# Kernel optimization log

Measured on AMD Instinct MI355X. Metric: run time of the kernel, lower is better.

## Reference

```python
import jax, jax.numpy as jnp
import numpy as np

K = 5
PAD = 2


def setup_inputs() -> dict:
    key = jax.random.key(0)
    k1, k2 = jax.random.split(key)
    B, C, H, W = 8, 4, 256, 256
    x = jax.random.normal(k1, (B, C, H, W), dtype=jnp.float32)
    filt = jax.random.uniform(k2, (B, C * K * K, H, W), dtype=jnp.float32)
    return {"x": x, "filt": filt}


def reference(x, filt):
    B, C, H, W = x.shape
    # identity kernel: out channel j of each group picks the j-th position of the kxk window
    eye = jnp.eye(K * K, dtype=x.dtype).reshape(K * K, 1, K, K)
    kernel = jnp.tile(eye, (C, 1, 1, 1))  # [C*K^2, 1, K, K], grouped conv = per-channel patch expand
    x_localexpand = jax.lax.conv_general_dilated(
        x, kernel,
        window_strides=(1, 1),
        padding=[(PAD, PAD), (PAD, PAD)],
        dimension_numbers=("NCHW", "OIHW", "NCHW"),
        feature_group_count=C,
    )  # [B, C*K^2, H, W]
    y = jnp.tanh(jnp.sum(x_localexpand * filt, axis=1, keepdims=True))  # [B,1,H,W]
    return y
```

## Files before the change

kernel.cpp:

```cpp
#include <hip/hip_runtime.h>
#include <math.h>

#define Hd 256
#define Wd 256
#define Cc 4
#define Kk 5

__global__ __launch_bounds__(256) void dynf_kernel(const float* __restrict__ x,
                                                   const float* __restrict__ filt,
                                                   float* __restrict__ out) {
    int t  = blockIdx.x * blockDim.x + threadIdx.x;
    int w4 = t & 63;
    int h  = (t >> 6) & 255;
    int b  = t >> 14;
    int w0 = w4 << 2;

    const size_t HW = (size_t)Hd * Wd;
    const float* xb = x + (size_t)b * Cc * HW;
    const float* fb = filt + (size_t)b * (Cc * Kk * Kk) * HW;

    float acc0 = 0.f, acc1 = 0.f, acc2 = 0.f, acc3 = 0.f;

    for (int c = 0; c < Cc; ++c) {
        const float* xc = xb + (size_t)c * HW;
        #pragma unroll
        for (int di = 0; di < Kk; ++di) {
            int hh = h + di - 2;
            if (hh < 0 || hh >= Hd) continue;
            const float* xr = xc + (size_t)hh * Wd;

            float4 left  = (w0 >= 4)      ? *(const float4*)(xr + w0 - 4) : make_float4(0.f,0.f,0.f,0.f);
            float4 mid   =                  *(const float4*)(xr + w0);
            float4 right = (w0 + 4 < Wd)  ? *(const float4*)(xr + w0 + 4) : make_float4(0.f,0.f,0.f,0.f);
            float xrow[8];
            xrow[0] = left.z;  xrow[1] = left.w;
            xrow[2] = mid.x;   xrow[3] = mid.y;  xrow[4] = mid.z;  xrow[5] = mid.w;
            xrow[6] = right.x; xrow[7] = right.y;

            const float* fr = fb + ((size_t)(c * (Kk*Kk) + di * Kk)) * HW + (size_t)h * Wd + w0;
            #pragma unroll
            for (int dj = 0; dj < Kk; ++dj) {
                float4 f = *(const float4*)(fr + (size_t)dj * HW);
                acc0 = fmaf(xrow[dj + 0], f.x, acc0);
                acc1 = fmaf(xrow[dj + 1], f.y, acc1);
                acc2 = fmaf(xrow[dj + 2], f.z, acc2);
                acc3 = fmaf(xrow[dj + 3], f.w, acc3);
            }
        }
    }

    float4 o;
    o.x = tanhf(acc0); o.y = tanhf(acc1); o.z = tanhf(acc2); o.w = tanhf(acc3);
    *(float4*)(out + (size_t)b * HW + (size_t)h * Wd + w0) = o;
}

extern "C" void kernel_launch(void* const* d_in, const int* in_sizes, int n_in,
                              void* d_out, int out_size, void* d_ws, size_t ws_size,
                              hipStream_t stream) {
    const float* x    = (const float*)d_in[0];
    const float* filt = (const float*)d_in[1];
    float* out        = (float*)d_out;

    const int total_threads = 8 * 256 * 64;
    const int block = 256;
    const int grid  = total_threads / block;
    dynf_kernel<<<grid, block, 0, stream>>>(x, filt, out);
}
```

Baseline: 286.3 us.

## Split channels across waves per row block and reduce via shared memory

```diff
diff --git a/kernel.cpp b/kernel.cpp
--- a/kernel.cpp
+++ b/kernel.cpp
@@ -4,54 +4,63 @@
 #define Hd 256
 #define Wd 256
 #define Cc 4
-#define Kk 5
+#define KK 5
 
-__global__ __launch_bounds__(256) void dynf_kernel(const float* __restrict__ x,
-                                                   const float* __restrict__ filt,
-                                                   float* __restrict__ out) {
-    int t  = blockIdx.x * blockDim.x + threadIdx.x;
-    int w4 = t & 63;
-    int h  = (t >> 6) & 255;
-    int b  = t >> 14;
-    int w0 = w4 << 2;
+typedef float v4f __attribute__((ext_vector_type(4)));
+
+__global__ __launch_bounds__(256, 4) void dynf_kernel(const float* __restrict__ x,
+                                                      const float* __restrict__ filt,
+                                                      float* __restrict__ out) {
+    const int bh   = blockIdx.x;
+    const int b    = bh >> 8;
+    const int h    = bh & 255;
+    const int c    = threadIdx.x >> 6;
+    const int lane = threadIdx.x & 63;
+    const int w0   = lane << 2;
 
     const size_t HW = (size_t)Hd * Wd;
-    const float* xb = x + (size_t)b * Cc * HW;
-    const float* fb = filt + (size_t)b * (Cc * Kk * Kk) * HW;
+    const float* xc = x + ((size_t)b * Cc + c) * HW;
+    const float* fb = filt + ((size_t)(b * (Cc * KK * KK) + c * (KK * KK))) * HW
+                      + (size_t)h * Wd + w0;
 
-    float acc0 = 0.f, acc1 = 0.f, acc2 = 0.f, acc3 = 0.f;
+    float a0 = 0.f, a1 = 0.f, a2 = 0.f, a3 = 0.f;
+    const v4f vzero = {0.f, 0.f, 0.f, 0.f};
 
-    for (int c = 0; c < Cc; ++c) {
-        const float* xc = xb + (size_t)c * HW;
-        #pragma unroll
-        for (int di = 0; di < Kk; ++di) {
-            int hh = h + di - 2;
-            if (hh < 0 || hh >= Hd) continue;
+    #pragma unroll
+    for (int di = 0; di < KK; ++di) {
+        const int hh = h + di - 2;
+        if (hh >= 0 && hh < Hd) {
             const float* xr = xc + (size_t)hh * Wd;
+            v4f left  = *(const v4f*)(xr + (w0 ? (w0 - 4) : 0));
+            v4f mid   = *(const v4f*)(xr + w0);
+            v4f right = *(const v4f*)(xr + ((w0 + 4 < Wd) ? (w0 + 4) : 0));
+            if (w0 == 0)      left  = vzero;
+            if (w0 + 4 >= Wd) right = vzero;
+            float xrow[8] = {left.z, left.w, mid.x, mid.y, mid.z, mid.w, right.x, right.y};
 
-            float4 left  = (w0 >= 4)      ? *(const float4*)(xr + w0 - 4) : make_float4(0.f,0.f,0.f,0.f);
-            float4 mid   =                  *(const float4*)(xr + w0);
-            float4 right = (w0 + 4 < Wd)  ? *(const float4*)(xr + w0 + 4) : make_float4(0.f,0.f,0.f,0.f);
-            float xrow[8];
-            xrow[0] = left.z;  xrow[1] = left.w;
-            xrow[2] = mid.x;   xrow[3] = mid.y;  xrow[4] = mid.z;  xrow[5] = mid.w;
-            xrow[6] = right.x; xrow[7] = right.y;
-
-            const float* fr = fb + ((size_t)(c * (Kk*Kk) + di * Kk)) * HW + (size_t)h * Wd + w0;
+            const float* fr = fb + (size_t)(di * KK) * HW;
             #pragma unroll
-            for (int dj = 0; dj < Kk; ++dj) {
-                float4 f = *(const float4*)(fr + (size_t)dj * HW);
-                acc0 = fmaf(xrow[dj + 0], f.x, acc0);
-                acc1 = fmaf(xrow[dj + 1], f.y, acc1);
-                acc2 = fmaf(xrow[dj + 2], f.z, acc2);
-                acc3 = fmaf(xrow[dj + 3], f.w, acc3);
+            for (int dj = 0; dj < KK; ++dj) {
+                v4f f = __builtin_nontemporal_load((const v4f*)(fr + (size_t)dj * HW));
+                a0 = fmaf(xrow[dj + 0], f.x, a0);
+                a1 = fmaf(xrow[dj + 1], f.y, a1);
+                a2 = fmaf(xrow[dj + 2], f.z, a2);
+                a3 = fmaf(xrow[dj + 3], f.w, a3);
             }
         }
     }
 
-    float4 o;
-    o.x = tanhf(acc0); o.y = tanhf(acc1); o.z = tanhf(acc2); o.w = tanhf(acc3);
-    *(float4*)(out + (size_t)b * HW + (size_t)h * Wd + w0) = o;
+    __shared__ v4f red[Cc][64];
+    v4f acc = {a0, a1, a2, a3};
+    red[c][lane] = acc;
+    __syncthreads();
+
+    if (c == 0) {
+        v4f s = red[0][lane] + red[1][lane] + red[2][lane] + red[3][lane];
+        v4f o;
+        o.x = tanhf(s.x); o.y = tanhf(s.y); o.z = tanhf(s.z); o.w = tanhf(s.w);
+        __builtin_nontemporal_store(o, (v4f*)(out + (size_t)b * HW + (size_t)h * Wd + w0));
+    }
 }
 
 extern "C" void kernel_launch(void* const* d_in, const int* in_sizes, int n_in,
@@ -61,8 +70,7 @@
     const float* filt = (const float*)d_in[1];
     float* out        = (float*)d_out;
 
-    const int total_threads = 8 * 256 * 64;
+    const int grid  = 8 * 256;
     const int block = 256;
-    const int grid  = total_threads / block;
     dynf_kernel<<<grid, block, 0, stream>>>(x, filt, out);
 }
```

Measured after the change: 274.0 us. 4.3% less time.
